# Performance work log

Measured on AMD Instinct MI355X. Metric: run time of the kernel, lower is better.

Reference implementation:

```python
import jax, jax.numpy as jnp
import numpy as np

DIM = 768
TIME_DIM = 768
NUM_HEADS = 12
NUM_PATCHES = 784
GRID = 28  # sqrt(NUM_PATCHES)
REL_MAX = 2 * GRID - 1  # 55


def _rel_pos_indices():
    # Faithful to the torch buffer: relative_position_index = (dh + g-1) + (dw + g-1)
    coords = np.stack(np.meshgrid(np.arange(GRID), np.arange(GRID), indexing='ij'))  # [2,g,g]
    cf = coords.reshape(2, -1)  # [2,N]
    rel = cf[:, :, None] - cf[:, None, :]  # [2,N,N]
    rel = rel.transpose(1, 2, 0)
    rel[:, :, 0] += GRID - 1
    rel[:, :, 1] += GRID - 1
    idx = rel.sum(-1)  # [N,N], values in [0, 2*(2g-2)]
    # forward then splits this summed index (as written in the source):
    ih = idx // REL_MAX
    iw = idx % REL_MAX
    return jnp.asarray(ih, jnp.int32), jnp.asarray(iw, jnp.int32)


def setup_inputs() -> dict:
    key = jax.random.key(0)
    ks = jax.random.split(key, 16)
    B = 8
    s = 0.02
    inp = {
        'x_s': jax.random.normal(ks[0], (B, NUM_PATCHES, DIM), jnp.float32),
        'x_t': jax.random.normal(ks[1], (B, TIME_DIM), jnp.float32),
        'Wqs': jax.random.normal(ks[2], (DIM, DIM), jnp.float32) * s,
        'Wqt': jax.random.normal(ks[3], (TIME_DIM, DIM), jnp.float32) * s,
        'Wks': jax.random.normal(ks[4], (DIM, DIM), jnp.float32) * s,
        'Wkt': jax.random.normal(ks[5], (TIME_DIM, DIM), jnp.float32) * s,
        'Wvs': jax.random.normal(ks[6], (DIM, DIM), jnp.float32) * s,
        'Wvt': jax.random.normal(ks[7], (TIME_DIM, DIM), jnp.float32) * s,
        'rpb_table': jax.random.normal(ks[8], (REL_MAX, REL_MAX, NUM_HEADS), jnp.float32) * s,
        'proj_w': jax.random.normal(ks[9], (DIM, DIM), jnp.float32) * s,
        'proj_b': jnp.zeros((DIM,), jnp.float32),
    }
    return inp


def reference(x_s, x_t, Wqs, Wqt, Wks, Wkt, Wvs, Wvt, rpb_table, proj_w, proj_b):
    B, N, D = x_s.shape
    H = NUM_HEADS
    hd = D // H
    scale = hd ** -0.5

    # time-embed fused QKV: q = x_s @ Wqs + x_t @ Wqt (broadcast over tokens)
    q = x_s @ Wqs + (x_t @ Wqt)[:, None, :]
    k = x_s @ Wks + (x_t @ Wkt)[:, None, :]
    v = x_s @ Wvs + (x_t @ Wvt)[:, None, :]

    q = q.reshape(B, N, H, hd).transpose(0, 2, 1, 3)  # [B,H,N,hd]
    k = k.reshape(B, N, H, hd).transpose(0, 2, 1, 3)
    v = v.reshape(B, N, H, hd).transpose(0, 2, 1, 3)

    attn = jnp.einsum('bhnd,bhmd->bhnm', q, k) * scale  # [B,H,N,N]

    ih, iw = _rel_pos_indices()  # [N,N] each
    bias = rpb_table[ih, iw]  # [N,N,H]
    attn = attn + bias.transpose(2, 0, 1)[None]  # [1,H,N,N]

    attn = jax.nn.softmax(attn, axis=-1)
    x = jnp.einsum('bhnm,bhmd->bhnd', attn, v)
    x = x.transpose(0, 2, 1, 3).reshape(B, N, D)
    return x @ proj_w + proj_b
```

## Files before the change

### kernel.cpp

```cpp
#include <hip/hip_runtime.h>
#include <hip/hip_bf16.h>
#include <stdint.h>

#define DIM 768
#define NP  784
#define NH  12
#define HD  64
#define BATCH 8
#define MROWS (BATCH*NP)
#define MPAD 832
#define NCHUNK 32
#define KCH 24
#define L2E 1.4426950408889634f

using bf16x8 = __attribute__((ext_vector_type(8))) short;
using bf16x4 = __attribute__((ext_vector_type(4))) short;
using f32x4  = __attribute__((ext_vector_type(4))) float;

__device__ __forceinline__ short f2bf(float f) {
  union { float f; uint32_t u; } c; c.f = f;
  uint32_t u = c.u;
  u += 0x7FFFu + ((u >> 16) & 1u);
  return (short)(u >> 16);
}

__device__ __forceinline__ short bfr(float x) {
  union { __hip_bfloat16 b; short s; } u;
  u.b = __float2bfloat16(x);
  return u.s;
}

__device__ __forceinline__ void gld_lds16(const void* g, void* l) {
  __builtin_amdgcn_global_load_lds((const __attribute__((address_space(1))) uint32_t*)g,
                                   (__attribute__((address_space(3))) uint32_t*)l,
                                   16, 0, 0);
}

__global__ __launch_bounds__(256) void cvt_bf16_kernel(const float* __restrict__ src,
                                                       short* __restrict__ dst, int n8) {
  int i = blockIdx.x * 256 + threadIdx.x;
  if (i >= n8) return;
  const float4* s = (const float4*)src;
  float4 a = s[2*i], b = s[2*i+1];
  bf16x8 o;
  o[0]=f2bf(a.x); o[1]=f2bf(a.y); o[2]=f2bf(a.z); o[3]=f2bf(a.w);
  o[4]=f2bf(b.x); o[5]=f2bf(b.y); o[6]=f2bf(b.z); o[7]=f2bf(b.w);
  ((bf16x8*)dst)[i] = o;
}

__global__ __launch_bounds__(256) void wtrans_kernel(const float* __restrict__ w0,
                                                     const float* __restrict__ w1,
                                                     const float* __restrict__ w2,
                                                     const float* __restrict__ w3,
                                                     short* __restrict__ dst) {
  __shared__ float tile[32][33];
  const int z = blockIdx.z;
  const float* src = (z==0) ? w0 : (z==1) ? w1 : (z==2) ? w2 : w3;
  short* d = dst + (size_t)z * DIM * DIM;
  const int n0 = blockIdx.x*32, k0 = blockIdx.y*32;
  const int tx = threadIdx.x, ty = threadIdx.y;
#pragma unroll
  for (int i=0;i<4;i++) tile[ty+i*8][tx] = src[(size_t)(k0+ty+i*8)*DIM + n0+tx];
  __syncthreads();
#pragma unroll
  for (int i=0;i<4;i++) d[(size_t)(n0+ty+i*8)*DIM + k0+tx] = f2bf(tile[tx][ty+i*8]);
}

__global__ __launch_bounds__(256) void tvec1_kernel(const float* __restrict__ x_t,
                                                    const float* __restrict__ wq,
                                                    const float* __restrict__ wk,
                                                    const float* __restrict__ wv,
                                                    float* __restrict__ part) {
  const int z = blockIdx.x, kc = blockIdx.y;
  const float* w = (z==0) ? wq : (z==1) ? wk : wv;
  const int d = threadIdx.x;
  __shared__ float xs[BATCH][KCH];
  if (threadIdx.x < BATCH*KCH)
    xs[threadIdx.x / KCH][threadIdx.x % KCH] =
        x_t[(size_t)(threadIdx.x / KCH)*DIM + kc*KCH + threadIdx.x % KCH];
  __syncthreads();
  float a0[BATCH] = {}, a1[BATCH] = {}, a2[BATCH] = {};
#pragma unroll 4
  for (int k = 0; k < KCH; ++k) {
    const float* wr = w + (size_t)(kc*KCH + k)*DIM + d;
    float w0 = wr[0], w1 = wr[256], w2 = wr[512];
#pragma unroll
    for (int b = 0; b < BATCH; ++b) {
      float xv = xs[b][k];
      a0[b] += xv*w0; a1[b] += xv*w1; a2[b] += xv*w2;
    }
  }
#pragma unroll
  for (int b = 0; b < BATCH; ++b) {
    float* p = part + (((size_t)z*NCHUNK + kc)*BATCH + b)*DIM + d;
    p[0] = a0[b]; p[256] = a1[b]; p[512] = a2[b];
  }
}

__global__ __launch_bounds__(256) void tvec2_kernel(const float* __restrict__ part,
                                                    float* __restrict__ t) {
  const int i = blockIdx.x*256 + threadIdx.x;
  if (i >= 3*BATCH*DIM) return;
  const int z = i / (BATCH*DIM), rem = i % (BATCH*DIM);
  float s = 0.f;
#pragma unroll 8
  for (int c = 0; c < NCHUNK; ++c)
    s += part[((size_t)z*NCHUNK + c)*BATCH*DIM + rem];
  t[i] = s;
}

__global__ __launch_bounds__(512, 1) void qkv256_kernel(const short* __restrict__ A,
                                                        const short* __restrict__ Wt,
                                                        const float* __restrict__ aux,
                                                        short* __restrict__ outq,
                                                        short* __restrict__ outk,
                                                        short* __restrict__ outv) {
  __shared__ short As0[256*64];
  __shared__ short As1[256*64];
  __shared__ short Bs0[256*64];
  __shared__ short Bs1[256*64];
  const int bx = blockIdx.x, by = blockIdx.y;
  const int z = bx / 3;
  const int n0z = (bx - z*3) * 256;
  const short* Bz = Wt + (size_t)z * DIM * DIM;
  const int m0 = by * 256;
  const int tid = threadIdx.x, w = tid >> 6, lane = tid & 63;
  const int wr = w >> 2, wc = w & 3, ln15 = lane & 15, lg = lane >> 4;

  const int lr8 = lane >> 3, c8e = (lane & 7) * 8;
  const int swe = c8e ^ (lr8 << 3);
  const short* aS = A  + (size_t)(m0  + w*8 + lr8) * DIM + swe;
  const short* bS = Bz + (size_t)(n0z + w*8 + lr8) * DIM + swe;

#define STG2(DA, DB, TT) { \
    char* da_ = (char*)(DA) + w*1024; \
    char* db_ = (char*)(DB) + w*1024; \
    const int kk_ = (TT)*64; \
    gld_lds16(aS + (size_t)0*64*DIM + kk_, da_ + 0*8192); \
    gld_lds16(bS + (size_t)0*64*DIM + kk_, db_ + 0*8192); \
    gld_lds16(aS + (size_t)1*64*DIM + kk_, da_ + 1*8192); \
    gld_lds16(bS + (size_t)1*64*DIM + kk_, db_ + 1*8192); \
    gld_lds16(aS + (size_t)2*64*DIM + kk_, da_ + 2*8192); \
    gld_lds16(bS + (size_t)2*64*DIM + kk_, db_ + 2*8192); \
    gld_lds16(aS + (size_t)3*64*DIM + kk_, da_ + 3*8192); \
    gld_lds16(bS + (size_t)3*64*DIM + kk_, db_ + 3*8192); }

#define QBODY(AB, BB) { \
    _Pragma("unroll") \
    for (int ks = 0; ks < 2; ++ks) { \
      bf16x8 bfv[4]; \
      _Pragma("unroll") \
      for (int ni = 0; ni < 4; ++ni) { \
        const int row_ = wc*64 + ni*16 + ln15; \
        bfv[ni] = *(const bf16x8*)&(BB)[row_*64 + ((ks*32 + lg*8) ^ ((row_ & 7) << 3))]; \
      } \
      _Pragma("unroll") \
      for (int mi = 0; mi < 8; ++mi) { \
        const int row_ = wr*128 + mi*16 + ln15; \
        bf16x8 afv = *(const bf16x8*)&(AB)[row_*64 + ((ks*32 + lg*8) ^ ((row_ & 7) << 3))]; \
        _Pragma("unroll") \
        for (int ni = 0; ni < 4; ++ni) \
          acc[mi][ni] = __builtin_amdgcn_mfma_f32_16x16x32_bf16(afv, bfv[ni], acc[mi][ni], 0,0,0); \
      } \
    } }

  f32x4 acc[8][4] = {};

  STG2(As0, Bs0, 0)
  STG2(As1, Bs1, 1)

  for (int tt = 0; tt < 5; ++tt) {
    const int t2 = tt*2;
    asm volatile("s_waitcnt vmcnt(8)" ::: "memory");
    __builtin_amdgcn_s_barrier();
    QBODY(As0, Bs0)
    __builtin_amdgcn_s_barrier();
    STG2(As0, Bs0, t2+2)
    asm volatile("s_waitcnt vmcnt(8)" ::: "memory");
    __builtin_amdgcn_s_barrier();
    QBODY(As1, Bs1)
    __builtin_amdgcn_s_barrier();
    STG2(As1, Bs1, t2+3)
  }
  asm volatile("s_waitcnt vmcnt(8)" ::: "memory");
  __builtin_amdgcn_s_barrier();
  QBODY(As0, Bs0)
  __builtin_amdgcn_s_barrier();
  asm volatile("s_waitcnt vmcnt(0)" ::: "memory");
  __builtin_amdgcn_s_barrier();
  QBODY(As1, Bs1)

  const float scl = 0.125f * L2E;
#pragma unroll
  for (int ai = 0; ai < 8; ++ai) {
    const int rb = m0 + wr*128 + (ai>>2)*64 + (ai&3)*16 + lg*4;
    if (z == 2) {
      if (rb < MROWS) {
        const int bb = rb / NP;
        const int m  = rb - bb*NP;
        const float* tv = aux + ((size_t)2*BATCH + bb) * DIM;
#pragma unroll
        for (int ni = 0; ni < 4; ++ni) {
          const int col = n0z + wc*64 + ni*16 + ln15;
          const int h = col >> 6, d = col & 63;
          const float tb = tv[col];
          bf16x4 ov;
          ov[0] = f2bf(acc[ai][ni][0] + tb);
          ov[1] = f2bf(acc[ai][ni][1] + tb);
          ov[2] = f2bf(acc[ai][ni][2] + tb);
          ov[3] = f2bf(acc[ai][ni][3] + tb);
          *(bf16x4*)&outv[((size_t)(bb*NH + h)*HD + d)*MPAD + m] = ov;
        }
      }
    } else {
#pragma unroll
      for (int j = 0; j < 4; ++j) {
        const int r = rb + j;
        if (r < MROWS) {
          const int bb = r / NP;
          const int m  = r - bb*NP;
          const float* tv = aux + ((size_t)z*BATCH + bb) * DIM;
#pragma unroll
          for (int ni = 0; ni < 4; ++ni) {
            const int col = n0z + wc*64 + ni*16 + ln15;
            if (z == 0) {
              outq[(size_t)r*DIM + col] = f2bf((acc[ai][ni][j] + tv[col]) * scl);
            } else {
              const int h = col >> 6, d = col & 63;
              outk[((size_t)(bb*NH + h)*MPAD + m)*HD + d] = f2bf(acc[ai][ni][j] + tv[col]);
            }
          }
        }
      }
    }
  }
#undef STG2
#undef QBODY
}

template<int MODE>
__global__ __launch_bounds__(256) void gemm_kernel(const short* __restrict__ A,
                                                   const short* __restrict__ Bw,
                                                   const float* __restrict__ aux,
                                                   float* __restrict__ outf) {
  __shared__ short As[128*32];
  __shared__ short Bs[128*32];
  const int bx = blockIdx.x, by = blockIdx.y;
  const short* Bz = Bw;
  const int tid = threadIdx.x, w = tid>>6, lane = tid&63;
  const int wr = w>>1, wc = w&1, ln15 = lane&15, lg = lane>>4;
  const int m0 = by*128, n0 = bx*128;

  f32x4 acc[4][4] = {};

  for (int kt=0; kt<24; ++kt) {
    const int k0 = kt*32;
    __syncthreads();
#pragma unroll
    for (int i=0;i<2;i++) {
      const int inst = w*2 + i;
      const int off  = inst*1024 + lane*16;
      const int row  = off >> 6;
      const int ce   = (off & 63) >> 1;
      gld_lds16(A  + (size_t)(m0+row)*DIM + k0 + ce, (char*)As + (size_t)inst*1024);
      gld_lds16(Bz + (size_t)(n0+row)*DIM + k0 + ce, (char*)Bs + (size_t)inst*1024);
    }
    __syncthreads();
    bf16x8 af[4], bfr_[4];
#pragma unroll
    for (int mi=0;mi<4;mi++) af[mi]   = *(const bf16x8*)&As[(wr*64+mi*16+ln15)*32 + lg*8];
#pragma unroll
    for (int ni=0;ni<4;ni++) bfr_[ni] = *(const bf16x8*)&Bs[(wc*64+ni*16+ln15)*32 + lg*8];
#pragma unroll
    for (int mi=0;mi<4;mi++)
#pragma unroll
      for (int ni=0;ni<4;ni++)
        acc[mi][ni] = __builtin_amdgcn_mfma_f32_16x16x32_bf16(af[mi], bfr_[ni], acc[mi][ni], 0,0,0);
  }

#pragma unroll
  for (int mi=0;mi<4;mi++)
#pragma unroll
    for (int j=0;j<4;j++) {
      const int r = m0 + wr*64 + mi*16 + lg*4 + j;
#pragma unroll
      for (int ni=0;ni<4;ni++) {
        const int gcol = n0 + wc*64 + ni*16 + ln15;
        outf[(size_t)r*DIM + gcol] = acc[mi][ni][j] + aux[gcol];
      }
    }
}

__global__ __launch_bounds__(512) void attn6_kernel(const short* __restrict__ Qb,
                                                    const short* __restrict__ Kt,
                                                    const short* __restrict__ Vt,
                                                    const float* __restrict__ rpb,
                                                    short* __restrict__ Ob) {
  __shared__ short kt[2][4096];
  __shared__ short vt[2][4096];
  __shared__ float4 bias4[112];
  const int hw = blockIdx.x;
  const int lgid = (hw & 7) * 84 + (hw >> 3);
  const int qt = lgid % 7;
  const int bh = lgid / 7;
  const int h = bh % NH, b = bh / NH;
  const int q0 = qt*128, tid = threadIdx.x, w = tid >> 6, lane = tid & 63;
  const int ln15 = lane & 15, lg = lane >> 4;

  if (tid < 112) {
    float4 v;
#pragma unroll
    for (int j = 0; j < 4; ++j) {
      const int i = tid - j - 2;
      float bv = 0.f;
      if (i >= 0 && i < 109)
        bv = rpb[(i/55)*(55*NH) + (i%55)*NH + h] * L2E;
      ((float*)&v)[j] = bv;
    }
    bias4[tid] = v;
  }

  const bool active = (q0 + w*16) < NP;
  const int q_idx = q0 + w*16 + ln15;
  bf16x8 qf0 = {}, qf1 = {};
  if (active) {
    const short* qp = Qb + ((size_t)(b*NP) + q_idx)*DIM + h*HD + lg*8;
    qf0 = *(const bf16x8*)qp;
    qf1 = *(const bf16x8*)(qp + 32);
  }
  const int qs56 = q_idx/28 + q_idx%28 + 56;

  const int lr = lane >> 3, lc = lane & 7;
  const int swe = (lc ^ lr) << 3;
  const size_t bhs = (size_t)bh;
  const short* kp0 = Kt + (bhs*MPAD + (size_t)(w*8 + lr))*HD + swe;
  const short* vp0 = Vt + (bhs*HD + (size_t)(w*8 + lr))*MPAD + swe;

#define STAGE2(BUF) { \
    gld_lds16(kp0, (char*)kt[BUF] + w*1024); \
    gld_lds16(vp0, (char*)vt[BUF] + w*1024); \
    kp0 += 64*HD; vp0 += 64; }

  float l_part = 0.f;
  f32x4 o0 = {}, o1 = {}, o2 = {}, o3 = {};

  STAGE2(0)

  for (int t = 0; t < 13; ++t) {
    const int cur = t & 1;
    const int m0 = t * 64;
    __syncthreads();
    if (t < 12) STAGE2(cur^1)
    if (active) {
      const char* kb = (const char*)kt[cur];
      const int sw = (ln15 & 7) << 4;
      f32x4 s[4];
#pragma unroll
      for (int mc = 0; mc < 4; ++mc) {
        const int rb = (mc*16 + ln15) * 128;
        bf16x8 kf0 = *(const bf16x8*)(kb + rb + ((lg*16) ^ sw));
        bf16x8 kf1 = *(const bf16x8*)(kb + rb + ((lg*16 + 64) ^ sw));
        f32x4 a = {};
        a = __builtin_amdgcn_mfma_f32_16x16x32_bf16(kf0, qf0, a, 0,0,0);
        a = __builtin_amdgcn_mfma_f32_16x16x32_bf16(kf1, qf1, a, 0,0,0);
        s[mc] = a;
      }
#pragma unroll
      for (int mc = 0; mc < 4; ++mc) {
        const int mb = m0 + mc*16 + lg*4;
        const int a28 = (mb * 2341) >> 16;
        const int idx0 = qs56 - mb + 27*a28;
        const float4 b4 = bias4[idx0];
        s[mc][0] += b4.x;
        s[mc][1] += b4.y;
        s[mc][2] += b4.z;
        s[mc][3] += b4.w;
      }
      if (m0 + 64 > NP) {
#pragma unroll
        for (int mc = 0; mc < 4; ++mc)
#pragma unroll
          for (int j = 0; j < 4; ++j)
            if (m0 + mc*16 + lg*4 + j >= NP) s[mc][j] = -1e30f;
      }
      float ts = 0.f;
      bf16x4 pb[4];
#pragma unroll
      for (int mc = 0; mc < 4; ++mc) {
        float p0 = exp2f(s[mc][0]), p1 = exp2f(s[mc][1]);
        float p2 = exp2f(s[mc][2]), p3 = exp2f(s[mc][3]);
        ts += (p0+p1)+(p2+p3);
        pb[mc][0] = bfr(p0); pb[mc][1] = bfr(p1);
        pb[mc][2] = bfr(p2); pb[mc][3] = bfr(p3);
      }
      l_part += ts;
      const char* vb = (const char*)vt[cur];
#pragma unroll
      for (int mc = 0; mc < 4; ++mc) {
        const int ib = (mc*32 + lg*8) ^ sw;
        bf16x4 vf0 = *(const bf16x4*)(vb + (0*16+ln15)*128 + ib);
        bf16x4 vf1 = *(const bf16x4*)(vb + (1*16+ln15)*128 + ib);
        bf16x4 vf2 = *(const bf16x4*)(vb + (2*16+ln15)*128 + ib);
        bf16x4 vf3 = *(const bf16x4*)(vb + (3*16+ln15)*128 + ib);
        o0 = __builtin_amdgcn_mfma_f32_16x16x16bf16_1k(vf0, pb[mc], o0, 0,0,0);
        o1 = __builtin_amdgcn_mfma_f32_16x16x16bf16_1k(vf1, pb[mc], o1, 0,0,0);
        o2 = __builtin_amdgcn_mfma_f32_16x16x16bf16_1k(vf2, pb[mc], o2, 0,0,0);
        o3 = __builtin_amdgcn_mfma_f32_16x16x16bf16_1k(vf3, pb[mc], o3, 0,0,0);
      }
    }
  }
#undef STAGE2

  if (active) {
    float l = l_part;
    l += __shfl_xor(l, 16);
    l += __shfl_xor(l, 32);
    const float inv = 1.0f / l;
    short* op = Ob + ((size_t)(b*NP) + q_idx)*DIM + h*HD + lg*4;
    bf16x4 ov;
    ov[0]=bfr(o0[0]*inv); ov[1]=bfr(o0[1]*inv); ov[2]=bfr(o0[2]*inv); ov[3]=bfr(o0[3]*inv);
    *(bf16x4*)(op + 0*16) = ov;
    ov[0]=bfr(o1[0]*inv); ov[1]=bfr(o1[1]*inv); ov[2]=bfr(o1[2]*inv); ov[3]=bfr(o1[3]*inv);
    *(bf16x4*)(op + 1*16) = ov;
    ov[0]=bfr(o2[0]*inv); ov[1]=bfr(o2[1]*inv); ov[2]=bfr(o2[2]*inv); ov[3]=bfr(o2[3]*inv);
    *(bf16x4*)(op + 2*16) = ov;
    ov[0]=bfr(o3[0]*inv); ov[1]=bfr(o3[1]*inv); ov[2]=bfr(o3[2]*inv); ov[3]=bfr(o3[3]*inv);
    *(bf16x4*)(op + 3*16) = ov;
  }
}

extern "C" void kernel_launch(void* const* d_in, const int* in_sizes, int n_in,
                              void* d_out, int out_size, void* d_ws, size_t ws_size,
                              hipStream_t stream) {
  const float* x_s = (const float*)d_in[0];
  const float* x_t = (const float*)d_in[1];
  const float* Wqs = (const float*)d_in[2];
  const float* Wqt = (const float*)d_in[3];
  const float* Wks = (const float*)d_in[4];
  const float* Wkt = (const float*)d_in[5];
  const float* Wvs = (const float*)d_in[6];
  const float* Wvt = (const float*)d_in[7];
  const float* rpb = (const float*)d_in[8];
  const float* pw  = (const float*)d_in[9];
  const float* pb  = (const float*)d_in[10];
  float* out = (float*)d_out;

  char* ws = (char*)d_ws;
  size_t off = 0;
  float* t_part = (float*)(ws + off); off += (size_t)3*NCHUNK*BATCH*DIM*4;
  float* t_vec  = (float*)(ws + off); off += (size_t)3*BATCH*DIM*4;
  short* Wt     = (short*)(ws + off); off += (size_t)4*DIM*DIM*2;
  short* Qb     = (short*)(ws + off); off += (size_t)MROWS*DIM*2;
  short* Ob     = (short*)(ws + off); off += (size_t)MROWS*DIM*2;
  short* Xb     = (short*)(ws + off); off += (size_t)(MROWS+256)*DIM*2;
  short* Kt     = (short*)(ws + off); off += (size_t)BATCH*NH*MPAD*HD*2;
  short* Vt     = (short*)(ws + off); off += (size_t)BATCH*NH*MPAD*HD*2;

  cvt_bf16_kernel<<<2352, 256, 0, stream>>>(x_s, Xb, MROWS*DIM/8);
  wtrans_kernel<<<dim3(24,24,4), dim3(32,8), 0, stream>>>(Wqs, Wks, Wvs, pw, Wt);
  tvec1_kernel<<<dim3(3,NCHUNK), 256, 0, stream>>>(x_t, Wqt, Wkt, Wvt, t_part);
  tvec2_kernel<<<72, 256, 0, stream>>>(t_part, t_vec);
  qkv256_kernel<<<dim3(9,25), 512, 0, stream>>>(Xb, Wt, t_vec, Qb, Kt, Vt);
  attn6_kernel<<<672, 512, 0, stream>>>(Qb, Kt, Vt, rpb, Ob);
  gemm_kernel<1><<<dim3(6,49,1), 256, 0, stream>>>(Ob, Wt + (size_t)3*DIM*DIM, pb, out);
}
```

Measured before the change: 129.7 us.

## Process two query tiles per wave in attention, halving block threads

The attention kernel now runs 4 waves of 256 threads instead of 8 waves, and each wave handles two 16-row query groups (A and B, 64 rows apart). Each K and V fragment read from shared memory is reused for both groups, which halves LDS reads per MFMA. Each wave now issues two staging loads for K and two for V. The cost is roughly double the accumulator and score registers per wave and fewer waves per block, which reduces latency hiding. A launch-bounds hint of 3 blocks per CU is added.

```diff
diff --git a/kernel.cpp b/kernel.cpp
--- a/kernel.cpp
+++ b/kernel.cpp
@@ -291,11 +291,11 @@
     }
 }
 
-__global__ __launch_bounds__(512) void attn6_kernel(const short* __restrict__ Qb,
-                                                    const short* __restrict__ Kt,
-                                                    const short* __restrict__ Vt,
-                                                    const float* __restrict__ rpb,
-                                                    short* __restrict__ Ob) {
+__global__ __launch_bounds__(256, 3) void attn7_kernel(const short* __restrict__ Qb,
+                                                       const short* __restrict__ Kt,
+                                                       const short* __restrict__ Vt,
+                                                       const float* __restrict__ rpb,
+                                                       short* __restrict__ Ob) {
   __shared__ short kt[2][4096];
   __shared__ short vt[2][4096];
   __shared__ float4 bias4[112];
@@ -320,80 +320,99 @@
     bias4[tid] = v;
   }
 
-  const bool active = (q0 + w*16) < NP;
-  const int q_idx = q0 + w*16 + ln15;
-  bf16x8 qf0 = {}, qf1 = {};
-  if (active) {
-    const short* qp = Qb + ((size_t)(b*NP) + q_idx)*DIM + h*HD + lg*8;
-    qf0 = *(const bf16x8*)qp;
-    qf1 = *(const bf16x8*)(qp + 32);
-  }
-  const int qs56 = q_idx/28 + q_idx%28 + 56;
+  const bool actA = (q0 + w*16) < NP;
+  const bool actB = (q0 + 64 + w*16) < NP;
+  const int qA = q0 + w*16 + ln15;
+  const int qB = qA + 64;
+  bf16x8 qfA0 = {}, qfA1 = {}, qfB0 = {}, qfB1 = {};
+  if (actA) {
+    const short* qp = Qb + ((size_t)(b*NP) + qA)*DIM + h*HD + lg*8;
+    qfA0 = *(const bf16x8*)qp;
+    qfA1 = *(const bf16x8*)(qp + 32);
+  }
+  if (actB) {
+    const short* qp = Qb + ((size_t)(b*NP) + qB)*DIM + h*HD + lg*8;
+    qfB0 = *(const bf16x8*)qp;
+    qfB1 = *(const bf16x8*)(qp + 32);
+  }
+  const int qs56A = qA/28 + qA%28 + 56;
+  const int qs56B = qB/28 + qB%28 + 56;
 
   const int lr = lane >> 3, lc = lane & 7;
   const int swe = (lc ^ lr) << 3;
   const size_t bhs = (size_t)bh;
-  const short* kp0 = Kt + (bhs*MPAD + (size_t)(w*8 + lr))*HD + swe;
-  const short* vp0 = Vt + (bhs*HD + (size_t)(w*8 + lr))*MPAD + swe;
-
-#define STAGE2(BUF) { \
-    gld_lds16(kp0, (char*)kt[BUF] + w*1024); \
-    gld_lds16(vp0, (char*)vt[BUF] + w*1024); \
-    kp0 += 64*HD; vp0 += 64; }
-
-  float l_part = 0.f;
-  f32x4 o0 = {}, o1 = {}, o2 = {}, o3 = {};
-
-  STAGE2(0)
+  const short* kp0 = Kt + (bhs*MPAD + (size_t)(w*16 + lr))*HD + swe;
+  const short* kp1 = kp0 + 8*HD;
+  const short* vp0 = Vt + (bhs*HD + (size_t)(w*16 + lr))*MPAD + swe;
+  const short* vp1 = vp0 + 8*MPAD;
+
+#define STAGE4(BUF) { \
+    gld_lds16(kp0, (char*)kt[BUF] + w*2048); \
+    gld_lds16(kp1, (char*)kt[BUF] + w*2048 + 1024); \
+    gld_lds16(vp0, (char*)vt[BUF] + w*2048); \
+    gld_lds16(vp1, (char*)vt[BUF] + w*2048 + 1024); \
+    kp0 += 64*HD; kp1 += 64*HD; vp0 += 64; vp1 += 64; }
+
+  float lA = 0.f, lB = 0.f;
+  f32x4 oA0={}, oA1={}, oA2={}, oA3={};
+  f32x4 oB0={}, oB1={}, oB2={}, oB3={};
+
+  STAGE4(0)
 
   for (int t = 0; t < 13; ++t) {
     const int cur = t & 1;
     const int m0 = t * 64;
     __syncthreads();
-    if (t < 12) STAGE2(cur^1)
-    if (active) {
+    if (t < 12) STAGE4(cur^1)
+    if (actA || actB) {
       const char* kb = (const char*)kt[cur];
       const int sw = (ln15 & 7) << 4;
-      f32x4 s[4];
+      f32x4 sA[4], sB[4];
 #pragma unroll
       for (int mc = 0; mc < 4; ++mc) {
         const int rb = (mc*16 + ln15) * 128;
         bf16x8 kf0 = *(const bf16x8*)(kb + rb + ((lg*16) ^ sw));
         bf16x8 kf1 = *(const bf16x8*)(kb + rb + ((lg*16 + 64) ^ sw));
         f32x4 a = {};
-        a = __builtin_amdgcn_mfma_f32_16x16x32_bf16(kf0, qf0, a, 0,0,0);
-        a = __builtin_amdgcn_mfma_f32_16x16x32_bf16(kf1, qf1, a, 0,0,0);
-        s[mc] = a;
+        a = __builtin_amdgcn_mfma_f32_16x16x32_bf16(kf0, qfA0, a, 0,0,0);
+        a = __builtin_amdgcn_mfma_f32_16x16x32_bf16(kf1, qfA1, a, 0,0,0);
+        sA[mc] = a;
+        f32x4 c = {};
+        c = __builtin_amdgcn_mfma_f32_16x16x32_bf16(kf0, qfB0, c, 0,0,0);
+        c = __builtin_amdgcn_mfma_f32_16x16x32_bf16(kf1, qfB1, c, 0,0,0);
+        sB[mc] = c;
       }
 #pragma unroll
       for (int mc = 0; mc < 4; ++mc) {
         const int mb = m0 + mc*16 + lg*4;
         const int a28 = (mb * 2341) >> 16;
-        const int idx0 = qs56 - mb + 27*a28;
-        const float4 b4 = bias4[idx0];
-        s[mc][0] += b4.x;
-        s[mc][1] += b4.y;
-        s[mc][2] += b4.z;
-        s[mc][3] += b4.w;
+        const int rel = 27*a28 - mb;
+        const float4 bA = bias4[qs56A + rel];
+        const float4 bB = bias4[qs56B + rel];
+        sA[mc][0] += bA.x; sA[mc][1] += bA.y; sA[mc][2] += bA.z; sA[mc][3] += bA.w;
+        sB[mc][0] += bB.x; sB[mc][1] += bB.y; sB[mc][2] += bB.z; sB[mc][3] += bB.w;
       }
       if (m0 + 64 > NP) {
 #pragma unroll
         for (int mc = 0; mc < 4; ++mc)
 #pragma unroll
           for (int j = 0; j < 4; ++j)
-            if (m0 + mc*16 + lg*4 + j >= NP) s[mc][j] = -1e30f;
-      }
-      float ts = 0.f;
-      bf16x4 pb[4];
+            if (m0 + mc*16 + lg*4 + j >= NP) { sA[mc][j] = -1e30f; sB[mc][j] = -1e30f; }
+      }
+      float tsA = 0.f, tsB = 0.f;
+      bf16x4 pbA[4], pbB[4];
 #pragma unroll
       for (int mc = 0; mc < 4; ++mc) {
-        float p0 = exp2f(s[mc][0]), p1 = exp2f(s[mc][1]);
-        float p2 = exp2f(s[mc][2]), p3 = exp2f(s[mc][3]);
-        ts += (p0+p1)+(p2+p3);
-        pb[mc][0] = bfr(p0); pb[mc][1] = bfr(p1);
-        pb[mc][2] = bfr(p2); pb[mc][3] = bfr(p3);
-      }
-      l_part += ts;
+        float a0 = exp2f(sA[mc][0]), a1 = exp2f(sA[mc][1]);
+        float a2 = exp2f(sA[mc][2]), a3 = exp2f(sA[mc][3]);
+        float b0 = exp2f(sB[mc][0]), b1 = exp2f(sB[mc][1]);
+        float b2 = exp2f(sB[mc][2]), b3 = exp2f(sB[mc][3]);
+        tsA += (a0+a1)+(a2+a3);
+        tsB += (b0+b1)+(b2+b3);
+        pbA[mc][0]=bfr(a0); pbA[mc][1]=bfr(a1); pbA[mc][2]=bfr(a2); pbA[mc][3]=bfr(a3);
+        pbB[mc][0]=bfr(b0); pbB[mc][1]=bfr(b1); pbB[mc][2]=bfr(b2); pbB[mc][3]=bfr(b3);
+      }
+      lA += tsA; lB += tsB;
       const char* vb = (const char*)vt[cur];
 #pragma unroll
       for (int mc = 0; mc < 4; ++mc) {
@@ -402,29 +421,49 @@
         bf16x4 vf1 = *(const bf16x4*)(vb + (1*16+ln15)*128 + ib);
         bf16x4 vf2 = *(const bf16x4*)(vb + (2*16+ln15)*128 + ib);
         bf16x4 vf3 = *(const bf16x4*)(vb + (3*16+ln15)*128 + ib);
-        o0 = __builtin_amdgcn_mfma_f32_16x16x16bf16_1k(vf0, pb[mc], o0, 0,0,0);
-        o1 = __builtin_amdgcn_mfma_f32_16x16x16bf16_1k(vf1, pb[mc], o1, 0,0,0);
-        o2 = __builtin_amdgcn_mfma_f32_16x16x16bf16_1k(vf2, pb[mc], o2, 0,0,0);
-        o3 = __builtin_amdgcn_mfma_f32_16x16x16bf16_1k(vf3, pb[mc], o3, 0,0,0);
+        oA0 = __builtin_amdgcn_mfma_f32_16x16x16bf16_1k(vf0, pbA[mc], oA0, 0,0,0);
+        oA1 = __builtin_amdgcn_mfma_f32_16x16x16bf16_1k(vf1, pbA[mc], oA1, 0,0,0);
+        oA2 = __builtin_amdgcn_mfma_f32_16x16x16bf16_1k(vf2, pbA[mc], oA2, 0,0,0);
+        oA3 = __builtin_amdgcn_mfma_f32_16x16x16bf16_1k(vf3, pbA[mc], oA3, 0,0,0);
+        oB0 = __builtin_amdgcn_mfma_f32_16x16x16bf16_1k(vf0, pbB[mc], oB0, 0,0,0);
+        oB1 = __builtin_amdgcn_mfma_f32_16x16x16bf16_1k(vf1, pbB[mc], oB1, 0,0,0);
+        oB2 = __builtin_amdgcn_mfma_f32_16x16x16bf16_1k(vf2, pbB[mc], oB2, 0,0,0);
+        oB3 = __builtin_amdgcn_mfma_f32_16x16x16bf16_1k(vf3, pbB[mc], oB3, 0,0,0);
       }
     }
   }
-#undef STAGE2
-
-  if (active) {
-    float l = l_part;
+#undef STAGE4
+
+  if (actA) {
+    float l = lA;
     l += __shfl_xor(l, 16);
     l += __shfl_xor(l, 32);
     const float inv = 1.0f / l;
-    short* op = Ob + ((size_t)(b*NP) + q_idx)*DIM + h*HD + lg*4;
+    short* op = Ob + ((size_t)(b*NP) + qA)*DIM + h*HD + lg*4;
     bf16x4 ov;
-    ov[0]=bfr(o0[0]*inv); ov[1]=bfr(o0[1]*inv); ov[2]=bfr(o0[2]*inv); ov[3]=bfr(o0[3]*inv);
+    ov[0]=bfr(oA0[0]*inv); ov[1]=bfr(oA0[1]*inv); ov[2]=bfr(oA0[2]*inv); ov[3]=bfr(oA0[3]*inv);
     *(bf16x4*)(op + 0*16) = ov;
-    ov[0]=bfr(o1[0]*inv); ov[1]=bfr(o1[1]*inv); ov[2]=bfr(o1[2]*inv); ov[3]=bfr(o1[3]*inv);
+    ov[0]=bfr(oA1[0]*inv); ov[1]=bfr(oA1[1]*inv); ov[2]=bfr(oA1[2]*inv); ov[3]=bfr(oA1[3]*inv);
     *(bf16x4*)(op + 1*16) = ov;
-    ov[0]=bfr(o2[0]*inv); ov[1]=bfr(o2[1]*inv); ov[2]=bfr(o2[2]*inv); ov[3]=bfr(o2[3]*inv);
+    ov[0]=bfr(oA2[0]*inv); ov[1]=bfr(oA2[1]*inv); ov[2]=bfr(oA2[2]*inv); ov[3]=bfr(oA2[3]*inv);
     *(bf16x4*)(op + 2*16) = ov;
-    ov[0]=bfr(o3[0]*inv); ov[1]=bfr(o3[1]*inv); ov[2]=bfr(o3[2]*inv); ov[3]=bfr(o3[3]*inv);
+    ov[0]=bfr(oA3[0]*inv); ov[1]=bfr(oA3[1]*inv); ov[2]=bfr(oA3[2]*inv); ov[3]=bfr(oA3[3]*inv);
+    *(bf16x4*)(op + 3*16) = ov;
+  }
+  if (actB) {
+    float l = lB;
+    l += __shfl_xor(l, 16);
+    l += __shfl_xor(l, 32);
+    const float inv = 1.0f / l;
+    short* op = Ob + ((size_t)(b*NP) + qB)*DIM + h*HD + lg*4;
+    bf16x4 ov;
+    ov[0]=bfr(oB0[0]*inv); ov[1]=bfr(oB0[1]*inv); ov[2]=bfr(oB0[2]*inv); ov[3]=bfr(oB0[3]*inv);
+    *(bf16x4*)(op + 0*16) = ov;
+    ov[0]=bfr(oB1[0]*inv); ov[1]=bfr(oB1[1]*inv); ov[2]=bfr(oB1[2]*inv); ov[3]=bfr(oB1[3]*inv);
+    *(bf16x4*)(op + 1*16) = ov;
+    ov[0]=bfr(oB2[0]*inv); ov[1]=bfr(oB2[1]*inv); ov[2]=bfr(oB2[2]*inv); ov[3]=bfr(oB2[3]*inv);
+    *(bf16x4*)(op + 2*16) = ov;
+    ov[0]=bfr(oB3[0]*inv); ov[1]=bfr(oB3[1]*inv); ov[2]=bfr(oB3[2]*inv); ov[3]=bfr(oB3[3]*inv);
     *(bf16x4*)(op + 3*16) = ov;
   }
 }
@@ -461,6 +500,6 @@
   tvec1_kernel<<<dim3(3,NCHUNK), 256, 0, stream>>>(x_t, Wqt, Wkt, Wvt, t_part);
   tvec2_kernel<<<72, 256, 0, stream>>>(t_part, t_vec);
   qkv256_kernel<<<dim3(9,25), 512, 0, stream>>>(Xb, Wt, t_vec, Qb, Kt, Vt);
-  attn6_kernel<<<672, 512, 0, stream>>>(Qb, Kt, Vt, rpb, Ob);
+  attn7_kernel<<<672, 256, 0, stream>>>(Qb, Kt, Vt, rpb, Ob);
   gemm_kernel<1><<<dim3(6,49,1), 256, 0, stream>>>(Ob, Wt + (size_t)3*DIM*DIM, pb, out);
 }
```

Result: no change. 129.7 us (-0.0%).
